# Kernel optimization log

Hardware: AMD Instinct MI355X
Metric: run time of the kernel (lower is better)

Reference implementation:

```python
import jax, jax.numpy as jnp
import numpy as np

B, S, D, H = 4, 2048, 1024, 16
DK = D // H

def setup_inputs() -> dict:
    key = jax.random.key(0)
    ks = jax.random.split(key, 11)
    sc = 1.0 / np.sqrt(D)
    return {
        "query": jax.random.normal(ks[0], (B, S, D), jnp.float32),
        "key": jax.random.normal(ks[1], (B, S, D), jnp.float32),
        "value": jax.random.normal(ks[2], (B, S, D), jnp.float32),
        "Wq": jax.random.normal(ks[3], (D, D), jnp.float32) * sc,
        "bq": jnp.zeros((D,), jnp.float32),
        "Wk": jax.random.normal(ks[4], (D, D), jnp.float32) * sc,
        "bk": jnp.zeros((D,), jnp.float32),
        "Wv": jax.random.normal(ks[5], (D, D), jnp.float32) * sc,
        "bv": jnp.zeros((D,), jnp.float32),
        "Wo": jax.random.normal(ks[6], (D, D), jnp.float32) * sc,
        "bo": jnp.zeros((D,), jnp.float32),
    }

def _mha(query, key, value, Wq, bq, Wk, bk, Wv, bv, Wo, bo):
    # in_linear{0,1,2}: y = x @ W.T + b  (MetaLinearLayer, weight [out,in])
    def proj(x, W, b):
        y = jnp.einsum('bsd,ed->bse', x, W) + b
        return y.reshape(B, S, H, DK).transpose(0, 2, 1, 3)  # [B,H,S,DK]
    q = proj(query, Wq, bq)
    k = proj(key, Wk, bk)
    v = proj(value, Wv, bv)
    # scores = QK^T / sqrt(d_k)  -> [B,H,S,S] (materialized as in original)
    scores = jnp.einsum('bhqd,bhkd->bhqk', q, k) / jnp.sqrt(jnp.float32(DK))
    p_attn = jax.nn.softmax(scores, axis=-1)
    # dropout is identity in eval/reference mode
    x = jnp.einsum('bhqk,bhkd->bhqd', p_attn, v)
    x = x.transpose(0, 2, 1, 3).reshape(B, S, D)
    return jnp.einsum('bsd,ed->bse', x, Wo) + bo

def reference(query, key, value, Wq, bq, Wk, bk, Wv, bv, Wo, bo):
    return _mha(query, key, value, Wq, bq, Wk, bk, Wv, bv, Wo, bo)
```

## Files before the change

kernel.cpp:

```cpp
#include <hip/hip_runtime.h>
#include <stdint.h>

typedef __attribute__((ext_vector_type(4))) float f32x4;
typedef __attribute__((ext_vector_type(8))) __bf16 bf16x8;
typedef __attribute__((ext_vector_type(8))) unsigned short u16x8;
typedef __attribute__((ext_vector_type(4))) uint32_t u32x4;

#define GLOBAL_AS __attribute__((address_space(1)))
#define LDS_AS    __attribute__((address_space(3)))

__device__ __forceinline__ void lds_load16(const void* g, void* l) {
  __builtin_amdgcn_global_load_lds((const GLOBAL_AS uint32_t*)(uintptr_t)g,
                                   (LDS_AS uint32_t*)(uintptr_t)l, 16, 0, 0);
}

__device__ __forceinline__ unsigned short f2bf(float f) {
  uint32_t u = __builtin_bit_cast(uint32_t, f);
  u += 0x7fffu + ((u >> 16) & 1u);
  return (unsigned short)(u >> 16);
}

__device__ __forceinline__ uint32_t pk_bf16(float a, float b) {
#if __has_builtin(__builtin_amdgcn_cvt_pk_bf16_f32)
  return __builtin_bit_cast(uint32_t, __builtin_amdgcn_cvt_pk_bf16_f32(a, b));
#else
  return (uint32_t)f2bf(a) | ((uint32_t)f2bf(b) << 16);
#endif
}

__device__ __forceinline__ float exp2f_fast(float x) {
#if __has_builtin(__builtin_amdgcn_exp2f)
  return __builtin_amdgcn_exp2f(x);
#else
  return __expf(x * 0.6931471805599453f);
#endif
}

__device__ __forceinline__ bf16x8 pack8(const f32x4 a, const f32x4 b) {
  u32x4 d;
  d.x = pk_bf16(a[0], a[1]);
  d.y = pk_bf16(a[2], a[3]);
  d.z = pk_bf16(b[0], b[1]);
  d.w = pk_bf16(b[2], b[3]);
  return __builtin_bit_cast(bf16x8, d);
}

__global__ void cast_all(const float* __restrict__ q, const float* __restrict__ k,
                         const float* __restrict__ v, const float* __restrict__ Wq,
                         const float* __restrict__ Wk, const float* __restrict__ Wv,
                         const float* __restrict__ Wo, unsigned short* __restrict__ dst) {
  const int bid = blockIdx.x;
  const float* src;
  int rel;
  if (bid < 24576) {
    const int seg = bid >> 13;
    rel = bid & 8191;
    src = (seg == 0) ? q : (seg == 1) ? k : v;
  } else {
    const int w = (bid - 24576) >> 10;
    rel = (bid - 24576) & 1023;
    src = (w == 0) ? Wq : (w == 1) ? Wk : (w == 2) ? Wv : Wo;
  }
  const size_t di = (size_t)bid * 1024 + threadIdx.x * 4;
  const size_t si = (size_t)rel * 1024 + threadIdx.x * 4;
  const float4 val = *(const float4*)(src + si);
  ushort4 o;
  o.x = f2bf(val.x); o.y = f2bf(val.y); o.z = f2bf(val.z); o.w = f2bf(val.w);
  *(ushort4*)(dst + di) = o;
}

__global__ __launch_bounds__(256, 2)
void gemm_qkv(const unsigned short* __restrict__ xq, const unsigned short* __restrict__ xk,
              const unsigned short* __restrict__ xv, const unsigned short* __restrict__ wq,
              const unsigned short* __restrict__ wk, const unsigned short* __restrict__ wv,
              const float* __restrict__ bq, const float* __restrict__ bk,
              const float* __restrict__ bv,
              unsigned short* __restrict__ Qh, unsigned short* __restrict__ Kh,
              unsigned short* __restrict__ Vt)
{
  __shared__ __align__(16) unsigned short As[128 * 32];
  __shared__ __align__(16) unsigned short Bs[128 * 32];

  const int gy = blockIdx.y, gx = blockIdx.x;
  const unsigned short* A  = (gy == 0) ? xq : (gy == 1) ? xk : wv;
  const unsigned short* Bw = (gy == 0) ? wq : (gy == 1) ? wk : xv;
  const float* bias        = (gy == 0) ? bq : (gy == 1) ? bk : bv;

  int m0, n0, N;
  if (gy < 2) { m0 = (gx >> 3) * 128; n0 = (gx & 7) * 128; N = 1024; }
  else        { m0 = (gx & 7) * 128;  n0 = (gx >> 3) * 128; N = 8192; }
  const int K = 1024;

  const int tid  = threadIdx.x;
  const int wave = tid >> 6;
  const int lane = tid & 63;
  const int wm = wave >> 1, wn = wave & 1;
  const int quad = lane >> 4, l15 = lane & 15;

  f32x4 acc[4][4];
#pragma unroll
  for (int i = 0; i < 4; ++i)
#pragma unroll
    for (int j = 0; j < 4; ++j) acc[i][j] = f32x4{0.f, 0.f, 0.f, 0.f};

  const int sr = lane >> 2;
  const int sc = (lane & 3) * 8;
  const unsigned short* Ag0 = A  + (size_t)(m0 + wave * 16 + sr) * K + sc;
  const unsigned short* Ag1 = Ag0 + (size_t)64 * K;
  const unsigned short* Bg0 = Bw + (size_t)(n0 + wave * 16 + sr) * K + sc;
  const unsigned short* Bg1 = Bg0 + (size_t)64 * K;
  unsigned short* AsW0 = &As[wave * 512];
  unsigned short* AsW1 = &As[2048 + wave * 512];
  unsigned short* BsW0 = &Bs[wave * 512];
  unsigned short* BsW1 = &Bs[2048 + wave * 512];

  for (int k0 = 0; k0 < K; k0 += 32) {
    lds_load16(Ag0 + k0, AsW0);
    lds_load16(Ag1 + k0, AsW1);
    lds_load16(Bg0 + k0, BsW0);
    lds_load16(Bg1 + k0, BsW1);
    __syncthreads();

    bf16x8 af[4], bfr[4];
#pragma unroll
    for (int i = 0; i < 4; ++i)
      af[i] = *(const bf16x8*)&As[(wm * 64 + i * 16 + l15) * 32 + quad * 8];
#pragma unroll
    for (int j = 0; j < 4; ++j)
      bfr[j] = *(const bf16x8*)&Bs[(wn * 64 + j * 16 + l15) * 32 + quad * 8];
#pragma unroll
    for (int i = 0; i < 4; ++i)
#pragma unroll
      for (int j = 0; j < 4; ++j)
        acc[i][j] = __builtin_amdgcn_mfma_f32_16x16x32_bf16(af[i], bfr[j], acc[i][j], 0, 0, 0);
    __syncthreads();
  }

  if (gy < 2) {
    unsigned short* out = (gy == 0) ? Qh : Kh;
    float bj[4];
#pragma unroll
    for (int j = 0; j < 4; ++j) bj[j] = bias[n0 + wn * 64 + j * 16 + l15];
#pragma unroll
    for (int i = 0; i < 4; ++i) {
      const int mbase = m0 + wm * 64 + i * 16 + quad * 4;
#pragma unroll
      for (int j = 0; j < 4; ++j) {
        const int n = n0 + wn * 64 + j * 16 + l15;
#pragma unroll
        for (int r = 0; r < 4; ++r) {
          const int m = mbase + r;
          const float vv = acc[i][j][r] + bj[j];
          const size_t idx = ((((size_t)(m >> 11) * 16 + (n >> 6)) << 11) + (size_t)(m & 2047)) * 64 + (n & 63);
          out[idx] = f2bf(vv);
        }
      }
    }
  } else {
#pragma unroll
    for (int i = 0; i < 4; ++i) {
      const int mbase = m0 + wm * 64 + i * 16 + quad * 4;
      float bm[4];
#pragma unroll
      for (int r = 0; r < 4; ++r) bm[r] = bias[mbase + r];
#pragma unroll
      for (int j = 0; j < 4; ++j) {
        const int n = n0 + wn * 64 + j * 16 + l15;
#pragma unroll
        for (int r = 0; r < 4; ++r)
          Vt[(size_t)(mbase + r) * N + n] = f2bf(acc[i][j][r] + bm[r]);
      }
    }
  }
}

__global__ __launch_bounds__(256, 2)
void flash_attn(const unsigned short* __restrict__ Qh,
                const unsigned short* __restrict__ Kh,
                const unsigned short* __restrict__ VtG,
                unsigned short* __restrict__ Xo)
{
  __shared__ __align__(16) unsigned short Ks[128 * 72];
  __shared__ __align__(16) unsigned short Vs[64 * 136];

  const int qb = blockIdx.x, h = blockIdx.y, b = blockIdx.z;
  const int tid = threadIdx.x, wave = tid >> 6, lane = tid & 63;
  const int quad = lane >> 4, l15 = lane & 15;

  const size_t bh = (((size_t)b * 16 + h) << 17);
  const unsigned short* Qg = Qh + bh + ((size_t)qb << 13);
  const unsigned short* Kg = Kh + bh;
  const unsigned short* Vg = VtG + ((size_t)(h * 64)) * 8192 + (size_t)b * 2048;

#pragma unroll
  for (int p = 0; p < 4; ++p) {
    const int c = tid + p * 256;
    u16x8 qv = *(const u16x8*)(Qg + c * 8);
    *(u16x8*)&Ks[(c >> 3) * 72 + (c & 7) * 8] = qv;
  }
  __syncthreads();
  bf16x8 aq[2][2];
#pragma unroll
  for (int i = 0; i < 2; ++i)
#pragma unroll
    for (int d = 0; d < 2; ++d)
      aq[i][d] = *(const bf16x8*)&Ks[(wave * 32 + i * 16 + l15) * 72 + d * 32 + quad * 8];

  f32x4 oacc[2][4];
  float mrow[2], lrow[2];
#pragma unroll
  for (int i = 0; i < 2; ++i) {
#pragma unroll
    for (int jd = 0; jd < 4; ++jd) oacc[i][jd] = f32x4{0.f, 0.f, 0.f, 0.f};
    mrow[i] = -1e30f; lrow[i] = 0.f;
  }

  const int rb = (l15 >> 3) * 16 + ((l15 >> 2) & 1) * 4 + (l15 & 3);

  const float SCALE = 0.18033688011112042f;

  u16x8 kreg[4], vreg[4];
#pragma unroll
  for (int p = 0; p < 4; ++p) {
    const int c = tid + p * 256;
    kreg[p] = *(const u16x8*)(Kg + c * 8);
    vreg[p] = *(const u16x8*)(Vg + (size_t)(c >> 4) * 8192 + (c & 15) * 8);
  }

  for (int kb = 0; kb < 16; ++kb) {
    __syncthreads();
#pragma unroll
    for (int p = 0; p < 4; ++p) {
      const int c = tid + p * 256;
      const int kr = c >> 3;
      const int krp = (kr & ~12) | ((kr & 4) << 1) | ((kr & 8) >> 1);
      *(u16x8*)&Ks[krp * 72 + (c & 7) * 8] = kreg[p];
      *(u16x8*)&Vs[(c >> 4) * 136 + (c & 15) * 8] = vreg[p];
    }
    __syncthreads();

#pragma unroll 1
    for (int hh = 0; hh < 2; ++hh) {
      f32x4 s[2][4];
#pragma unroll
      for (int i = 0; i < 2; ++i)
#pragma unroll
        for (int j = 0; j < 4; ++j) s[i][j] = f32x4{0.f, 0.f, 0.f, 0.f};
#pragma unroll
      for (int d = 0; d < 2; ++d)
#pragma unroll
        for (int j = 0; j < 4; ++j) {
          const int kk = j >> 1, p2 = j & 1;
          bf16x8 kf = *(const bf16x8*)&Ks[(hh * 64 + kk * 32 + p2 * 8 + rb) * 72 + d * 32 + quad * 8];
#pragma unroll
          for (int i = 0; i < 2; ++i)
            s[i][j] = __builtin_amdgcn_mfma_f32_16x16x32_bf16(kf, aq[i][d], s[i][j], 0, 0, 0);
        }

#pragma unroll
      for (int i = 0; i < 2; ++i) {
        float mx = -1e30f;
#pragma unroll
        for (int j = 0; j < 4; ++j)
#pragma unroll
          for (int r = 0; r < 4; ++r) {
            s[i][j][r] *= SCALE;
            mx = fmaxf(mx, s[i][j][r]);
          }
        mx = fmaxf(mx, __shfl_xor(mx, 16));
        mx = fmaxf(mx, __shfl_xor(mx, 32));
        const float mo = mrow[i];
        const float mn = fmaxf(mo, mx);
        mrow[i] = mn;
        const float al = exp2f_fast(mo - mn);
        float rs = 0.f;
#pragma unroll
        for (int j = 0; j < 4; ++j)
#pragma unroll
          for (int r = 0; r < 4; ++r) {
            const float p = exp2f_fast(s[i][j][r] - mn);
            s[i][j][r] = p;
            rs += p;
          }
        rs += __shfl_xor(rs, 16);
        rs += __shfl_xor(rs, 32);
        lrow[i] = lrow[i] * al + rs;

#pragma unroll
        for (int r = 0; r < 4; ++r) {
          const float aO = __shfl(al, quad * 4 + r);
#pragma unroll
          for (int jd = 0; jd < 4; ++jd) oacc[i][jd][r] *= aO;
        }
      }

      bf16x8 ap[2][2];
#pragma unroll
      for (int i = 0; i < 2; ++i)
#pragma unroll
        for (int kk = 0; kk < 2; ++kk)
          ap[i][kk] = pack8(s[i][2 * kk], s[i][2 * kk + 1]);

      if (kb < 15) {
        if (hh == 0) {
          const size_t ko = ((size_t)(kb + 1) << 13);
#pragma unroll
          for (int p = 0; p < 4; ++p) {
            const int c = tid + p * 256;
            kreg[p] = *(const u16x8*)(Kg + ko + c * 8);
          }
        } else {
#pragma unroll
          for (int p = 0; p < 4; ++p) {
            const int c = tid + p * 256;
            vreg[p] = *(const u16x8*)(Vg + (size_t)(c >> 4) * 8192 + (kb + 1) * 128 + (c & 15) * 8);
          }
        }
      }

#pragma unroll
      for (int kk = 0; kk < 2; ++kk) {
#pragma unroll
        for (int jd = 0; jd < 4; ++jd) {
          bf16x8 bv = *(const bf16x8*)&Vs[(jd * 16 + l15) * 136 + (hh * 2 + kk) * 32 + quad * 8];
#pragma unroll
          for (int i = 0; i < 2; ++i)
            oacc[i][jd] = __builtin_amdgcn_mfma_f32_16x16x32_bf16(ap[i][kk], bv, oacc[i][jd], 0, 0, 0);
        }
      }
    }
  }

#pragma unroll
  for (int i = 0; i < 2; ++i)
#pragma unroll
    for (int r = 0; r < 4; ++r) {
      const float lO = __shfl(lrow[i], quad * 4 + r);
      const float inv = 1.f / lO;
      const int srow = qb * 128 + wave * 32 + i * 16 + quad * 4 + r;
      const size_t obase = (((size_t)b << 11) + srow) * 1024 + (h << 6);
#pragma unroll
      for (int jd = 0; jd < 4; ++jd)
        Xo[obase + jd * 16 + l15] = f2bf(oacc[i][jd][r] * inv);
    }
}

__global__ __launch_bounds__(256, 2)
void gemm_out(const unsigned short* __restrict__ A,
              const unsigned short* __restrict__ Bw,
              const float* __restrict__ bias,
              float* __restrict__ Cout)
{
  __shared__ __align__(16) unsigned short As[128 * 32];
  __shared__ __align__(16) unsigned short Bs[128 * 32];

  const int tid  = threadIdx.x;
  const int wave = tid >> 6;
  const int lane = tid & 63;
  const int wm = wave >> 1, wn = wave & 1;
  const int quad = lane >> 4, l15 = lane & 15;
  const int m0 = blockIdx.y * 128;
  const int n0 = blockIdx.x * 128;
  const int K = 1024, N = 1024;

  f32x4 acc[4][4];
#pragma unroll
  for (int i = 0; i < 4; ++i)
#pragma unroll
    for (int j = 0; j < 4; ++j) acc[i][j] = f32x4{0.f, 0.f, 0.f, 0.f};

  const int sr = lane >> 2;
  const int sc = (lane & 3) * 8;
  const unsigned short* Ag0 = A  + (size_t)(m0 + wave * 16 + sr) * K + sc;
  const unsigned short* Ag1 = Ag0 + (size_t)64 * K;
  const unsigned short* Bg0 = Bw + (size_t)(n0 + wave * 16 + sr) * K + sc;
  const unsigned short* Bg1 = Bg0 + (size_t)64 * K;
  unsigned short* AsW0 = &As[wave * 512];
  unsigned short* AsW1 = &As[2048 + wave * 512];
  unsigned short* BsW0 = &Bs[wave * 512];
  unsigned short* BsW1 = &Bs[2048 + wave * 512];

  for (int k0 = 0; k0 < K; k0 += 32) {
    lds_load16(Ag0 + k0, AsW0);
    lds_load16(Ag1 + k0, AsW1);
    lds_load16(Bg0 + k0, BsW0);
    lds_load16(Bg1 + k0, BsW1);
    __syncthreads();

    bf16x8 af[4], bfr[4];
#pragma unroll
    for (int i = 0; i < 4; ++i)
      af[i] = *(const bf16x8*)&As[(wm * 64 + i * 16 + l15) * 32 + quad * 8];
#pragma unroll
    for (int j = 0; j < 4; ++j)
      bfr[j] = *(const bf16x8*)&Bs[(wn * 64 + j * 16 + l15) * 32 + quad * 8];
#pragma unroll
    for (int i = 0; i < 4; ++i)
#pragma unroll
      for (int j = 0; j < 4; ++j)
        acc[i][j] = __builtin_amdgcn_mfma_f32_16x16x32_bf16(af[i], bfr[j], acc[i][j], 0, 0, 0);
    __syncthreads();
  }

  float bj[4];
#pragma unroll
  for (int j = 0; j < 4; ++j) bj[j] = bias[n0 + wn * 64 + j * 16 + l15];

#pragma unroll
  for (int i = 0; i < 4; ++i) {
    const int mbase = m0 + wm * 64 + i * 16 + quad * 4;
#pragma unroll
    for (int j = 0; j < 4; ++j) {
      const int n = n0 + wn * 64 + j * 16 + l15;
#pragma unroll
      for (int r = 0; r < 4; ++r)
        Cout[(size_t)(mbase + r) * N + n] = acc[i][j][r] + bj[j];
    }
  }
}

extern "C" void kernel_launch(void* const* d_in, const int* in_sizes, int n_in,
                              void* d_out, int out_size, void* d_ws, size_t ws_size,
                              hipStream_t stream) {
  const float* q  = (const float*)d_in[0];
  const float* k  = (const float*)d_in[1];
  const float* v  = (const float*)d_in[2];
  const float* Wq = (const float*)d_in[3];
  const float* bq = (const float*)d_in[4];
  const float* Wk = (const float*)d_in[5];
  const float* bk = (const float*)d_in[6];
  const float* Wv = (const float*)d_in[7];
  const float* bv = (const float*)d_in[8];
  const float* Wo = (const float*)d_in[9];
  const float* bo = (const float*)d_in[10];

  const int B = 4, S = 2048, D = 1024, H = 16;
  const size_t NX = (size_t)B * S * D;
  const size_t NW = (size_t)D * D;

  unsigned short* xq = (unsigned short*)d_ws;
  unsigned short* xk = xq + NX;
  unsigned short* xv = xk + NX;
  unsigned short* wq = xv + NX;
  unsigned short* wk = wq + NW;
  unsigned short* wv = wk + NW;
  unsigned short* wo = wv + NW;
  unsigned short* Qh = wo + NW;
  unsigned short* Kh = Qh + NX;
  unsigned short* Vt = Kh + NX;
  unsigned short* xo = Vt + NX;

  cast_all<<<28672, 256, 0, stream>>>(q, k, v, Wq, Wk, Wv, Wo, xq);
  gemm_qkv<<<dim3(512, 3), 256, 0, stream>>>(xq, xk, xv, wq, wk, wv, bq, bk, bv, Qh, Kh, Vt);
  flash_attn<<<dim3(S / 128, H, B), 256, 0, stream>>>(Qh, Kh, Vt, xo);
  gemm_out<<<dim3(D / 128, (B * S) / 128), 256, 0, stream>>>(xo, wo, bo, (float*)d_out);
}
```

Measured before the change: 408.2 us.

## Fold softmax scale into Q projection and skip rescale when max grows little

Multiplies the softmax scale (with log2e) into Q in the projection epilogue, so the attention inner loop drops its per-score multiply. Adds a lazy-rescale path: if every lane's block max stays within 8 of the running max, the running max is kept and the shuffles and output rescale are skipped. The row-sum shuffles are deferred to the end by keeping per-lane partial sums. This trims VALU and cross-lane work in the softmax at the cost of a wave-wide vote and branch, and exponents up to 2^8 before the final normalisation, a small precision risk.

```diff
diff --git a/kernel.cpp b/kernel.cpp
--- a/kernel.cpp
+++ b/kernel.cpp
@@ -44,6 +44,8 @@
   d.w = pk_bf16(b[2], b[3]);
   return __builtin_bit_cast(bf16x8, d);
 }
+
+#define QK_SCALE 0.18033688011112042f
 
 __global__ void cast_all(const float* __restrict__ q, const float* __restrict__ k,
                          const float* __restrict__ v, const float* __restrict__ Wq,
@@ -138,6 +140,7 @@
 
   if (gy < 2) {
     unsigned short* out = (gy == 0) ? Qh : Kh;
+    const float scl = (gy == 0) ? QK_SCALE : 1.0f;
     float bj[4];
 #pragma unroll
     for (int j = 0; j < 4; ++j) bj[j] = bias[n0 + wn * 64 + j * 16 + l15];
@@ -150,7 +153,7 @@
 #pragma unroll
         for (int r = 0; r < 4; ++r) {
           const int m = mbase + r;
-          const float vv = acc[i][j][r] + bj[j];
+          const float vv = (acc[i][j][r] + bj[j]) * scl;
           const size_t idx = ((((size_t)(m >> 11) * 16 + (n >> 6)) << 11) + (size_t)(m & 2047)) * 64 + (n & 63);
           out[idx] = f2bf(vv);
         }
@@ -207,17 +210,15 @@
       aq[i][d] = *(const bf16x8*)&Ks[(wave * 32 + i * 16 + l15) * 72 + d * 32 + quad * 8];
 
   f32x4 oacc[2][4];
-  float mrow[2], lrow[2];
+  float mrow[2], lpart[2];
 #pragma unroll
   for (int i = 0; i < 2; ++i) {
 #pragma unroll
     for (int jd = 0; jd < 4; ++jd) oacc[i][jd] = f32x4{0.f, 0.f, 0.f, 0.f};
-    mrow[i] = -1e30f; lrow[i] = 0.f;
+    mrow[i] = -1e30f; lpart[i] = 0.f;
   }
 
   const int rb = (l15 >> 3) * 16 + ((l15 >> 2) & 1) * 4 + (l15 & 3);
-
-  const float SCALE = 0.18033688011112042f;
 
   u16x8 kreg[4], vreg[4];
 #pragma unroll
@@ -263,34 +264,43 @@
 #pragma unroll
         for (int j = 0; j < 4; ++j)
 #pragma unroll
+          for (int r = 0; r < 4; ++r) mx = fmaxf(mx, s[i][j][r]);
+
+        if (__all(mx <= mrow[i] + 8.f)) {
+          const float mn = mrow[i];
+          float rs = 0.f;
+#pragma unroll
+          for (int j = 0; j < 4; ++j)
+#pragma unroll
+            for (int r = 0; r < 4; ++r) {
+              const float p = exp2f_fast(s[i][j][r] - mn);
+              s[i][j][r] = p;
+              rs += p;
+            }
+          lpart[i] += rs;
+        } else {
+          mx = fmaxf(mx, __shfl_xor(mx, 16));
+          mx = fmaxf(mx, __shfl_xor(mx, 32));
+          const float mo = mrow[i];
+          const float mn = fmaxf(mo, mx);
+          mrow[i] = mn;
+          const float al = exp2f_fast(mo - mn);
+          float rs = 0.f;
+#pragma unroll
+          for (int j = 0; j < 4; ++j)
+#pragma unroll
+            for (int r = 0; r < 4; ++r) {
+              const float p = exp2f_fast(s[i][j][r] - mn);
+              s[i][j][r] = p;
+              rs += p;
+            }
+          lpart[i] = lpart[i] * al + rs;
+#pragma unroll
           for (int r = 0; r < 4; ++r) {
-            s[i][j][r] *= SCALE;
-            mx = fmaxf(mx, s[i][j][r]);
+            const float aO = __shfl(al, quad * 4 + r);
+#pragma unroll
+            for (int jd = 0; jd < 4; ++jd) oacc[i][jd][r] *= aO;
           }
-        mx = fmaxf(mx, __shfl_xor(mx, 16));
-        mx = fmaxf(mx, __shfl_xor(mx, 32));
-        const float mo = mrow[i];
-        const float mn = fmaxf(mo, mx);
-        mrow[i] = mn;
-        const float al = exp2f_fast(mo - mn);
-        float rs = 0.f;
-#pragma unroll
-        for (int j = 0; j < 4; ++j)
-#pragma unroll
-          for (int r = 0; r < 4; ++r) {
-            const float p = exp2f_fast(s[i][j][r] - mn);
-            s[i][j][r] = p;
-            rs += p;
-          }
-        rs += __shfl_xor(rs, 16);
-        rs += __shfl_xor(rs, 32);
-        lrow[i] = lrow[i] * al + rs;
-
-#pragma unroll
-        for (int r = 0; r < 4; ++r) {
-          const float aO = __shfl(al, quad * 4 + r);
-#pragma unroll
-          for (int jd = 0; jd < 4; ++jd) oacc[i][jd][r] *= aO;
         }
       }
 
@@ -332,10 +342,13 @@
   }
 
 #pragma unroll
-  for (int i = 0; i < 2; ++i)
+  for (int i = 0; i < 2; ++i) {
+    float lf = lpart[i];
+    lf += __shfl_xor(lf, 16);
+    lf += __shfl_xor(lf, 32);
 #pragma unroll
     for (int r = 0; r < 4; ++r) {
-      const float lO = __shfl(lrow[i], quad * 4 + r);
+      const float lO = __shfl(lf, quad * 4 + r);
       const float inv = 1.f / lO;
       const int srow = qb * 128 + wave * 32 + i * 16 + quad * 4 + r;
       const size_t obase = (((size_t)b << 11) + srow) * 1024 + (h << 6);
@@ -343,6 +356,7 @@
       for (int jd = 0; jd < 4; ++jd)
         Xo[obase + jd * 16 + l15] = f2bf(oacc[i][jd][r] * inv);
     }
+  }
 }
 
 __global__ __launch_bounds__(256, 2)
```

After: 384.7 us. 1.06x faster.
